# Kernel optimization log

Hardware: AMD Instinct MI355X
Metric: run time of the kernel (lower is better)

Reference implementation:

```python
import jax, jax.numpy as jnp
import numpy as np

HEADS = 12


def setup_inputs() -> dict:
    key = jax.random.key(0)
    ks = jax.random.split(key, 3)
    B, N, C = 4, 2048, 768
    x = jax.random.normal(ks[0], (B, N, C), dtype=jnp.float32)
    Wqkv = jax.random.normal(ks[1], (C, 3 * C), dtype=jnp.float32) * 0.02
    bqkv = jnp.zeros((3 * C,), dtype=jnp.float32)
    Wproj = jax.random.normal(ks[2], (C, C), dtype=jnp.float32) * 0.02
    bproj = jnp.zeros((C,), dtype=jnp.float32)
    return {"x": x, "Wqkv": Wqkv, "bqkv": bqkv, "Wproj": Wproj, "bproj": bproj}


def reference(x, Wqkv, bqkv, Wproj, bproj):
    B, N, C = x.shape
    h = HEADS
    d = C // h
    scale = d ** (-0.5)
    # QKV projection: (B, N, 3C) -> (3, B, h, N, d)
    qkv = (x @ Wqkv + bqkv).reshape(B, N, 3, h, d).transpose(2, 0, 3, 1, 4)
    q, k, v = qkv[0], qkv[1], qkv[2]
    # Full N x N attention scores per head (matches original explicit matmul)
    scores = jnp.einsum("bhnd,bhmd->bhnm", q, k) * scale
    attn = jax.nn.softmax(scores, axis=-1)
    out = jnp.einsum("bhnm,bhmd->bhnd", attn, v)  # (B, h, N, d)
    out = out.transpose(0, 2, 1, 3).reshape(B, N, C)
    return out @ Wproj + bproj
```

## Files before the change

### kernel.cpp

```cpp
#include <hip/hip_runtime.h>
#include <hip/hip_bf16.h>
#include <math.h>

#define B_ 4
#define N_ 2048
#define C_ 768
#define H_ 12
#define D_ 64
#define SC_LOG2E 0.18033688f

typedef __attribute__((ext_vector_type(8))) short bf16x8;
typedef __attribute__((ext_vector_type(4))) float f32x4;

#define MFMA16(A, B, C) __builtin_amdgcn_mfma_f32_16x16x32_bf16(A, B, C, 0, 0, 0)

#if __has_builtin(__builtin_amdgcn_exp2f)
#define EXP2F(x) __builtin_amdgcn_exp2f(x)
#else
#define EXP2F(x) exp2f(x)
#endif

__device__ __forceinline__ ushort f2bf(float f) {
    union { float f; unsigned u; } v; v.f = f;
    unsigned r = v.u + 0x7fffu + ((v.u >> 16) & 1u);
    return (ushort)(r >> 16);
}

#if __has_builtin(__builtin_amdgcn_cvt_pk_bf16_f32)
typedef __attribute__((ext_vector_type(2))) __bf16 bf16x2v;
__device__ __forceinline__ unsigned pack_bf2(float a, float b) {
    union { bf16x2v v; unsigned u; } cv;
    cv.v = __builtin_amdgcn_cvt_pk_bf16_f32(a, b);
    return cv.u;
}
#else
__device__ __forceinline__ unsigned pack_bf2(float a, float b) {
    union { __hip_bfloat162 h2; unsigned u; } cv;
    cv.h2 = __float22bfloat162_rn(make_float2(a, b));
    return cv.u;
}
#endif

__device__ __forceinline__ void gl_lds16(const ushort* g, ushort* l) {
    __builtin_amdgcn_global_load_lds(
        (const __attribute__((address_space(1))) unsigned*)g,
        (__attribute__((address_space(3))) unsigned*)l, 16, 0, 0);
}

__device__ __forceinline__ void tr_body(const float* __restrict__ W,
                                        ushort* __restrict__ Wt,
                                        int K, int N, int bx, int by, int t) {
    __shared__ float T[32][33];
    int k0 = by * 32, n0 = bx * 32;
    int r = t >> 3, c4 = (t & 7) * 4;
    float4 v = *(const float4*)&W[(size_t)(k0 + r) * N + n0 + c4];
    T[r][c4] = v.x; T[r][c4 + 1] = v.y; T[r][c4 + 2] = v.z; T[r][c4 + 3] = v.w;
    __syncthreads();
    union { ushort s[4]; unsigned long long u; } o;
    o.s[0] = f2bf(T[c4 + 0][r]);
    o.s[1] = f2bf(T[c4 + 1][r]);
    o.s[2] = f2bf(T[c4 + 2][r]);
    o.s[3] = f2bf(T[c4 + 3][r]);
    *(unsigned long long*)&Wt[(size_t)(n0 + r) * K + k0 + c4] = o.u;
}

__global__ __launch_bounds__(256) void prep(
    const float* __restrict__ x, ushort* __restrict__ xb,
    const float* __restrict__ Wqkv, ushort* __restrict__ Wqkvt,
    const float* __restrict__ Wproj, ushort* __restrict__ Wprojt)
{
    const int bid = blockIdx.x, t = threadIdx.x;
    if (bid < 3072) {
        int i = bid * 256 + t;
        const float4* p = (const float4*)x + 2 * (size_t)i;
        float4 a = p[0], bq = p[1];
        union { ushort s[8]; uint4 v; } u;
        u.s[0] = f2bf(a.x);  u.s[1] = f2bf(a.y);  u.s[2] = f2bf(a.z);  u.s[3] = f2bf(a.w);
        u.s[4] = f2bf(bq.x); u.s[5] = f2bf(bq.y); u.s[6] = f2bf(bq.z); u.s[7] = f2bf(bq.w);
        *(uint4*)&xb[(size_t)i * 8] = u.v;
    } else if (bid < 4800) {
        int id = bid - 3072;
        tr_body(Wqkv, Wqkvt, C_, 3 * C_, id % 72, id / 72, t);
    } else {
        int id = bid - 4800;
        tr_body(Wproj, Wprojt, C_, C_, id % 24, id / 24, t);
    }
}

template <bool OBF>
__global__ __launch_bounds__(256) void gemm_bf16(
    const ushort* __restrict__ A, const ushort* __restrict__ Bt,
    const float* __restrict__ bias, void* __restrict__ outp,
    ushort* __restrict__ vtp,
    int M, int N, int K)
{
    __shared__ ushort Asl[128 * 64];
    __shared__ ushort Bsl[128 * 64];

    const int tid  = threadIdx.x;
    const int lane = tid & 63, w = tid >> 6;
    const int quad = lane >> 4, l16 = lane & 15;
    const int row0 = blockIdx.y * 128, col0 = blockIdx.x * 128;
    const int mh = (w >> 1) * 64, nh = (w & 1) * 64;

    f32x4 acc[4][4];
#pragma unroll
    for (int i = 0; i < 4; i++)
#pragma unroll
        for (int j = 0; j < 4; j++) acc[i][j] = (f32x4)0.f;

    for (int k0 = 0; k0 < K; k0 += 64) {
#pragma unroll
        for (int i = 0; i < 4; i++) {
            int c  = i * 256 + w * 64 + lane;
            int rr = c >> 3;
            int cc = (c & 7) ^ (rr & 7);
            int wb = (i * 256 + w * 64) * 8;
            gl_lds16(&A[(size_t)(row0 + rr) * K + k0 + cc * 8], &Asl[wb]);
            gl_lds16(&Bt[(size_t)(col0 + rr) * K + k0 + cc * 8], &Bsl[wb]);
        }
        __syncthreads();
#pragma unroll
        for (int h = 0; h < 2; h++) {
            const int sw = ((h * 4 + quad) ^ (l16 & 7)) * 8;
            bf16x8 af[4], bfr[4];
#pragma unroll
            for (int mt = 0; mt < 4; mt++)
                af[mt] = *(const bf16x8*)&Asl[(mh + mt * 16 + l16) * 64 + sw];
#pragma unroll
            for (int nt = 0; nt < 4; nt++)
                bfr[nt] = *(const bf16x8*)&Bsl[(nh + nt * 16 + l16) * 64 + sw];
#pragma unroll
            for (int mt = 0; mt < 4; mt++)
#pragma unroll
                for (int nt = 0; nt < 4; nt++)
                    acc[mt][nt] = MFMA16(af[mt], bfr[nt], acc[mt][nt]);
        }
        __syncthreads();
    }

    if (OBF && col0 >= 2 * C_) {
#pragma unroll
        for (int nt = 0; nt < 4; nt++) {
            int colh = col0 - 2 * C_ + nh + nt * 16 + l16;
            int hh = colh >> 6, dd = colh & 63;
            float bv = bias[col0 + nh + nt * 16 + l16];
#pragma unroll
            for (int mt = 0; mt < 4; mt++) {
                f32x4 v = acc[mt][nt];
                int row = row0 + mh + mt * 16 + quad * 4;
                int bb = row >> 11, tok = row & (N_ - 1);
                union { ushort us[4]; unsigned long long u; } o;
#pragma unroll
                for (int r = 0; r < 4; r++) o.us[r] = f2bf(v[r] + bv);
                *(unsigned long long*)&vtp[((size_t)(bb * H_ + hh) * D_ + dd) * N_ + tok] = o.u;
            }
        }
    } else {
        const float scl = (OBF && col0 < C_) ? SC_LOG2E : 1.f;
#pragma unroll
        for (int nt = 0; nt < 4; nt++) {
            int col = col0 + nh + nt * 16 + l16;
            float bv = bias[col];
#pragma unroll
            for (int mt = 0; mt < 4; mt++) {
                f32x4 v = acc[mt][nt];
#pragma unroll
                for (int r = 0; r < 4; r++) {
                    int row = row0 + mh + mt * 16 + quad * 4 + r;
                    if (OBF)
                        ((ushort*)outp)[(size_t)row * N + col] = f2bf((v[r] + bv) * scl);
                    else
                        ((float*)outp)[(size_t)row * N + col] = v[r] + bv;
                }
            }
        }
    }
}

__global__ __launch_bounds__(512, 6) void attn_mfma(
    const ushort* __restrict__ qkvb, const ushort* __restrict__ Vt,
    ushort* __restrict__ attnb)
{
    __shared__ ushort Kd[2][64 * 64];
    __shared__ ushort Vd[2][64 * 64];
    __shared__ ushort Ptl[8 * 16 * 72];

    const int tid  = threadIdx.x;
    const int lane = tid & 63, w = tid >> 6;
    const int quad = lane >> 4, l16 = lane & 15;

    const int flat = blockIdx.y * 16 + blockIdx.x;
    const int nf   = (flat & 7) * 96 + (flat >> 3);
    const int bh   = nf >> 4, qt_ = nf & 15;
    const int b = bh / H_, h = bh % H_;
    const int q0 = qt_ * 128 + w * 16;
    const size_t rowbase = (size_t)b * N_;
    const int hoff = h * D_;
    ushort* Ptw = Ptl + w * 16 * 72;
    const f32x4 Z4 = {0.f, 0.f, 0.f, 0.f};

    const ushort* Kg = qkvb + rowbase * (3 * C_) + C_ + hoff;
    const ushort* Vg = Vt + (size_t)bh * D_ * N_;

    const int rr = tid >> 3;
    const int cc = (tid & 7) ^ (rr & 7);
    const int wbase = w * 512;
    const ushort* kp = Kg + (size_t)rr * (3 * C_) + cc * 8;
    const ushort* vp = Vg + (size_t)rr * N_ + cc * 8;

    bf16x8 Qf[2];
#pragma unroll
    for (int c = 0; c < 2; c++)
        Qf[c] = *(const bf16x8*)&qkvb[(rowbase + q0 + l16) * (3 * C_)
                                      + hoff + c * 32 + quad * 8];

    f32x4 oacc[4];
#pragma unroll
    for (int dt = 0; dt < 4; dt++) oacc[dt] = (f32x4)0.f;
    float lrow = 0.f;

    const int NT = N_ / 64;
    gl_lds16(kp, &Kd[0][wbase]);
    gl_lds16(vp, &Vd[0][wbase]);
    kp += (size_t)64 * 3 * C_; vp += 64;
    asm volatile("s_waitcnt vmcnt(0)" ::: "memory");
    __builtin_amdgcn_s_barrier();
    __builtin_amdgcn_sched_barrier(0);

    for (int t = 0; t < NT; ++t) {
        const int rd = t & 1, wr = rd ^ 1;
        if (t + 1 < NT) {
            gl_lds16(kp, &Kd[wr][wbase]);
            gl_lds16(vp, &Vd[wr][wbase]);
            kp += (size_t)64 * 3 * C_; vp += 64;
        }
        __builtin_amdgcn_sched_barrier(0);

        const ushort* Kb = Kd[rd];
        const ushort* Vb = Vd[rd];

        f32x4 sacc[4];
        {
            bf16x8 kf[4];
#pragma unroll
            for (int kt = 0; kt < 4; kt++)
                kf[kt] = *(const bf16x8*)&Kb[(kt * 16 + l16) * 64
                                             + ((quad) ^ (l16 & 7)) * 8];
            __builtin_amdgcn_s_setprio(1);
#pragma unroll
            for (int kt = 0; kt < 4; kt++)
                sacc[kt] = MFMA16(kf[kt], Qf[0], Z4);
            __builtin_amdgcn_s_setprio(0);
        }
        {
            bf16x8 kf[4];
#pragma unroll
            for (int kt = 0; kt < 4; kt++)
                kf[kt] = *(const bf16x8*)&Kb[(kt * 16 + l16) * 64
                                             + ((4 | quad) ^ (l16 & 7)) * 8];
            __builtin_amdgcn_s_setprio(1);
#pragma unroll
            for (int kt = 0; kt < 4; kt++)
                sacc[kt] = MFMA16(kf[kt], Qf[1], sacc[kt]);
            __builtin_amdgcn_s_setprio(0);
        }

        {
            float sum = 0.f;
#pragma unroll
            for (int kt = 0; kt < 4; kt++) {
                float p0 = EXP2F(sacc[kt][0]);
                float p1 = EXP2F(sacc[kt][1]);
                float p2 = EXP2F(sacc[kt][2]);
                float p3 = EXP2F(sacc[kt][3]);
                sum += (p0 + p1) + (p2 + p3);
                uint2 pk;
                pk.x = pack_bf2(p0, p1);
                pk.y = pack_bf2(p2, p3);
                *(uint2*)&Ptw[l16 * 72 + kt * 16 + quad * 4] = pk;
            }
            lrow += sum;
        }

#pragma unroll
        for (int c = 0; c < 2; c++) {
            bf16x8 pf = *(const bf16x8*)&Ptw[l16 * 72 + c * 32 + quad * 8];
            __builtin_amdgcn_s_setprio(1);
#pragma unroll
            for (int dt = 0; dt < 4; dt++) {
                bf16x8 vf = *(const bf16x8*)&Vb[(dt * 16 + l16) * 64
                                   + (((c << 2) | quad) ^ (l16 & 7)) * 8];
                oacc[dt] = MFMA16(vf, pf, oacc[dt]);
            }
            __builtin_amdgcn_s_setprio(0);
        }

        asm volatile("s_waitcnt vmcnt(0)" ::: "memory");
        __builtin_amdgcn_s_barrier();
        __builtin_amdgcn_sched_barrier(0);
    }

    {
        float s = lrow;
        s += __shfl_xor(s, 16, 64);
        s += __shfl_xor(s, 32, 64);
        float inv = 1.f / s;
        size_t orow = (rowbase + q0 + l16) * C_ + hoff;
#pragma unroll
        for (int dt = 0; dt < 4; dt++) {
            union { ushort us[4]; unsigned long long u; } o;
#pragma unroll
            for (int r = 0; r < 4; r++) o.us[r] = f2bf(oacc[dt][r] * inv);
            *(unsigned long long*)&attnb[orow + dt * 16 + quad * 4] = o.u;
        }
    }
}

extern "C" void kernel_launch(void* const* d_in, const int* in_sizes, int n_in,
                              void* d_out, int out_size, void* d_ws, size_t ws_size,
                              hipStream_t stream)
{
    const float* x     = (const float*)d_in[0];
    const float* Wqkv  = (const float*)d_in[1];
    const float* bqkv  = (const float*)d_in[2];
    const float* Wproj = (const float*)d_in[3];
    const float* bproj = (const float*)d_in[4];

    ushort* xb     = (ushort*)d_ws;
    ushort* Wqkvt  = xb + (size_t)B_ * N_ * C_;
    ushort* Wprojt = Wqkvt + (size_t)3 * C_ * C_;
    ushort* qkvb   = Wprojt + (size_t)C_ * C_;
    ushort* attnb  = qkvb + (size_t)B_ * N_ * 3 * C_;
    ushort* Vtb    = attnb + (size_t)B_ * N_ * C_;

    const int M = B_ * N_;

    prep<<<5376, 256, 0, stream>>>(x, xb, Wqkv, Wqkvt, Wproj, Wprojt);

    gemm_bf16<true><<<dim3((3 * C_) / 128, M / 128), 256, 0, stream>>>(
        xb, Wqkvt, bqkv, qkvb, Vtb, M, 3 * C_, C_);

    attn_mfma<<<dim3(N_ / 128, B_ * H_), 512, 0, stream>>>(qkvb, Vtb, attnb);

    gemm_bf16<false><<<dim3(C_ / 128, M / 128), 256, 0, stream>>>(
        attnb, Wprojt, bproj, d_out, nullptr, M, C_, C_);
}
```

Baseline: 225.4 us.

## Keep softmax probabilities in registers and feed PV via 16x16x16 MFMA

The attention kernel no longer stages the exponentiated scores through a per-wave LDS tile. The packed bf16 P values stay in registers and serve directly as the A operand of 16x16x16 bf16 MFMAs against V read from LDS, which changes the output accumulator orientation. The epilogue now broadcasts each row's normalizer with shuffles and writes scalar bf16 stores. This removes an LDS write/read round trip and the shared buffer, but it doubles the number of MFMA issues for PV (half-K instructions) and makes the output stores narrower and less coalesced.

```diff
diff --git a/kernel.cpp b/kernel.cpp
--- a/kernel.cpp
+++ b/kernel.cpp
@@ -10,9 +10,22 @@
 #define SC_LOG2E 0.18033688f
 
 typedef __attribute__((ext_vector_type(8))) short bf16x8;
+typedef __attribute__((ext_vector_type(4))) short bf16x4;
 typedef __attribute__((ext_vector_type(4))) float f32x4;
 
 #define MFMA16(A, B, C) __builtin_amdgcn_mfma_f32_16x16x32_bf16(A, B, C, 0, 0, 0)
+
+#if __has_builtin(__builtin_amdgcn_mfma_f32_16x16x16bf16_1k)
+#define MFMA16K16(A, B, C) __builtin_amdgcn_mfma_f32_16x16x16bf16_1k(A, B, C, 0, 0, 0)
+#else
+__device__ __forceinline__ f32x4 mfma16k16_asm(bf16x4 a, bf16x4 b, f32x4 c) {
+    f32x4 d;
+    asm("v_mfma_f32_16x16x16_bf16 %0, %1, %2, %3"
+        : "=v"(d) : "v"(a), "v"(b), "v"(c));
+    return d;
+}
+#define MFMA16K16(A, B, C) mfma16k16_asm(A, B, C)
+#endif
 
 #if __has_builtin(__builtin_amdgcn_exp2f)
 #define EXP2F(x) __builtin_amdgcn_exp2f(x)
@@ -184,7 +197,6 @@
 {
     __shared__ ushort Kd[2][64 * 64];
     __shared__ ushort Vd[2][64 * 64];
-    __shared__ ushort Ptl[8 * 16 * 72];
 
     const int tid  = threadIdx.x;
     const int lane = tid & 63, w = tid >> 6;
@@ -197,7 +209,6 @@
     const int q0 = qt_ * 128 + w * 16;
     const size_t rowbase = (size_t)b * N_;
     const int hoff = h * D_;
-    ushort* Ptw = Ptl + w * 16 * 72;
     const f32x4 Z4 = {0.f, 0.f, 0.f, 0.f};
 
     const ushort* Kg = qkvb + rowbase * (3 * C_) + C_ + hoff;
@@ -217,7 +228,7 @@
 
     f32x4 oacc[4];
 #pragma unroll
-    for (int dt = 0; dt < 4; dt++) oacc[dt] = (f32x4)0.f;
+    for (int nt = 0; nt < 4; nt++) oacc[nt] = (f32x4)0.f;
     float lrow = 0.f;
 
     const int NT = N_ / 64;
@@ -266,6 +277,7 @@
             __builtin_amdgcn_s_setprio(0);
         }
 
+        unsigned pkx[4], pky[4];
         {
             float sum = 0.f;
 #pragma unroll
@@ -275,26 +287,26 @@
                 float p2 = EXP2F(sacc[kt][2]);
                 float p3 = EXP2F(sacc[kt][3]);
                 sum += (p0 + p1) + (p2 + p3);
-                uint2 pk;
-                pk.x = pack_bf2(p0, p1);
-                pk.y = pack_bf2(p2, p3);
-                *(uint2*)&Ptw[l16 * 72 + kt * 16 + quad * 4] = pk;
+                pkx[kt] = pack_bf2(p0, p1);
+                pky[kt] = pack_bf2(p2, p3);
             }
             lrow += sum;
         }
 
-#pragma unroll
-        for (int c = 0; c < 2; c++) {
-            bf16x8 pf = *(const bf16x8*)&Ptw[l16 * 72 + c * 32 + quad * 8];
-            __builtin_amdgcn_s_setprio(1);
-#pragma unroll
-            for (int dt = 0; dt < 4; dt++) {
-                bf16x8 vf = *(const bf16x8*)&Vb[(dt * 16 + l16) * 64
-                                   + (((c << 2) | quad) ^ (l16 & 7)) * 8];
-                oacc[dt] = MFMA16(vf, pf, oacc[dt]);
-            }
-            __builtin_amdgcn_s_setprio(0);
-        }
+        __builtin_amdgcn_s_setprio(1);
+#pragma unroll
+        for (int kt = 0; kt < 4; kt++) {
+            union { unsigned u[2]; bf16x4 s; } av;
+            av.u[0] = pkx[kt]; av.u[1] = pky[kt];
+            const int ch = ((kt * 2 + (quad >> 1)) ^ (l16 & 7));
+#pragma unroll
+            for (int nt = 0; nt < 4; nt++) {
+                bf16x4 vb = *(const bf16x4*)&Vb[(nt * 16 + l16) * 64
+                                                + ch * 8 + (quad & 1) * 4];
+                oacc[nt] = MFMA16K16(av.s, vb, oacc[nt]);
+            }
+        }
+        __builtin_amdgcn_s_setprio(0);
 
         asm volatile("s_waitcnt vmcnt(0)" ::: "memory");
         __builtin_amdgcn_s_barrier();
@@ -305,14 +317,17 @@
         float s = lrow;
         s += __shfl_xor(s, 16, 64);
         s += __shfl_xor(s, 32, 64);
-        float inv = 1.f / s;
-        size_t orow = (rowbase + q0 + l16) * C_ + hoff;
-#pragma unroll
-        for (int dt = 0; dt < 4; dt++) {
-            union { ushort us[4]; unsigned long long u; } o;
-#pragma unroll
-            for (int r = 0; r < 4; r++) o.us[r] = f2bf(oacc[dt][r] * inv);
-            *(unsigned long long*)&attnb[orow + dt * 16 + quad * 4] = o.u;
+        float invq[4];
+#pragma unroll
+        for (int r = 0; r < 4; r++)
+            invq[r] = 1.f / __shfl(s, quad * 4 + r, 64);
+#pragma unroll
+        for (int nt = 0; nt < 4; nt++) {
+#pragma unroll
+            for (int r = 0; r < 4; r++) {
+                size_t orow = (rowbase + q0 + quad * 4 + r) * C_ + hoff;
+                attnb[orow + nt * 16 + l16] = f2bf(oacc[nt][r] * invq[r]);
+            }
         }
     }
 }
```

Result: no change. 227.6 us (+1.0%).
